# Kernel tuning notes

Measured on AMD Instinct MI355X. Metric: run time of the kernel, lower is better.

Reference implementation:

```python
import jax, jax.numpy as jnp
import numpy as np

N = 2_000_000  # number of Gaussians


def setup_inputs() -> dict:
    key = jax.random.key(0)
    k1, k2, k3 = jax.random.split(key, 3)
    quaternions = jax.random.normal(k1, (N, 4), dtype=jnp.float32)
    scales = jax.random.normal(k2, (N, 3), dtype=jnp.float32) * 0.5
    opacities = jax.random.normal(k3, (N, 1), dtype=jnp.float32)
    return {"quaternions": quaternions, "scales": scales, "opacities": opacities}


def quaternion_to_rotation_matrix(q):
    # q: [N,4] with layout (w, x, y, z) as in the torch source
    w, x, y, z = q[:, 0], q[:, 1], q[:, 2], q[:, 3]
    xx, yy, zz = x * x, y * y, z * z
    xy, xz, yz = x * y, x * z, y * z
    xw, yw, zw = x * w, y * w, z * w
    r0 = jnp.stack([1 - 2 * (yy + zz), 2 * (xy - zw), 2 * (xz + yw)], axis=-1)
    r1 = jnp.stack([2 * (xy + zw), 1 - 2 * (xx + zz), 2 * (yz - xw)], axis=-1)
    r2 = jnp.stack([2 * (xz - yw), 2 * (yz + xw), 1 - 2 * (xx + yy)], axis=-1)
    return jnp.stack([r0, r1, r2], axis=-2)  # [N,3,3]


def reference(quaternions, scales, opacities):
    # sigmoid applied to raw opacities (source: 1/(1+exp(-o)))
    opac = jax.nn.sigmoid(opacities)
    # NOTE: source normalizes by the GLOBAL Frobenius norm of the whole tensor
    # (to.linalg.norm with no dim) -- replicated faithfully.
    qn = quaternions / jnp.linalg.norm(quaternions)
    R = quaternion_to_rotation_matrix(qn)  # [N,3,3]
    # scales_d = (diag(exp(s)))**2 ; scales_i_d = (diag(1/exp(s)))**2
    s2 = jnp.exp(2.0 * scales)      # [N,3] diagonal of S^2
    inv_s2 = jnp.exp(-2.0 * scales)  # [N,3] diagonal of S^-2
    # cov = R @ diag(s2) @ R^T, inv_cov = R @ diag(inv_s2) @ R^T (closed form,
    # no batched 3x3 matmul chain / LAPACK inverse needed)
    cov = jnp.einsum('nij,nj,nkj->nik', R, s2, R)
    inv_cov = jnp.einsum('nij,nj,nkj->nik', R, inv_s2, R)
    return cov, inv_cov, opac
```

## Files before the change

### kernel.cpp

```cpp
#include <hip/hip_runtime.h>
#include <math.h>

#define RBLOCKS 1024
#define RTHREADS 256
#define CHUNK 256

__global__ __launch_bounds__(RTHREADS) void gp_reduce_sq(
    const float4* __restrict__ q4, int n4, double* __restrict__ partials) {
    __shared__ double sdata[RTHREADS];
    double acc = 0.0;
    int stride = gridDim.x * blockDim.x;
    for (int i = blockIdx.x * blockDim.x + threadIdx.x; i < n4; i += stride) {
        float4 v = q4[i];
        acc += (double)v.x * v.x + (double)v.y * v.y +
               (double)v.z * v.z + (double)v.w * v.w;
    }
    sdata[threadIdx.x] = acc;
    __syncthreads();
    for (int s = RTHREADS / 2; s > 0; s >>= 1) {
        if (threadIdx.x < s) sdata[threadIdx.x] += sdata[threadIdx.x + s];
        __syncthreads();
    }
    if (threadIdx.x == 0) partials[blockIdx.x] = sdata[0];
}

__global__ __launch_bounds__(256) void gp_main(
    const float4* __restrict__ q,
    const float* __restrict__ scales,
    const float* __restrict__ opac_in,
    const double* __restrict__ partials,
    float* __restrict__ cov,
    float* __restrict__ inv_cov,
    float* __restrict__ opac_out,
    int n) {
    __shared__ union SU {
        double red[4];
        float mat[2 * CHUNK * 9];
    } u;
    __shared__ float s_sc[CHUNK * 3];

    const int tid = threadIdx.x;
    const int c0 = blockIdx.x * CHUNK;
    const int count = min(CHUNK, n - c0);

    float4 qi = make_float4(0.f, 0.f, 0.f, 0.f);
    float op = 0.f;
    if (tid < count) {
        qi = q[c0 + tid];
        op = opac_in[c0 + tid];
    }
    const int nsf = count * 3;
    const int nsf4 = nsf >> 2;
    const float4* sc4 = (const float4*)(scales + (size_t)c0 * 3);
    float4 sv = make_float4(0.f, 0.f, 0.f, 0.f);
    if (tid < nsf4) sv = sc4[tid];

    double acc = 0.0;
#pragma unroll
    for (int k = 0; k < RBLOCKS / 256; ++k) acc += partials[tid + 256 * k];
#pragma unroll
    for (int off = 32; off > 0; off >>= 1) acc += __shfl_down(acc, off);
    if ((tid & 63) == 0) u.red[tid >> 6] = acc;

    if (tid < nsf4) {
        s_sc[4 * tid + 0] = sv.x;
        s_sc[4 * tid + 1] = sv.y;
        s_sc[4 * tid + 2] = sv.z;
        s_sc[4 * tid + 3] = sv.w;
    }
    {
        int r = nsf - nsf4 * 4;
        if (tid < r) s_sc[nsf4 * 4 + tid] = scales[(size_t)c0 * 3 + nsf4 * 4 + tid];
    }
    __syncthreads();

    double tot = u.red[0] + u.red[1] + u.red[2] + u.red[3];
    const float inv_norm = (float)(1.0 / sqrt(tot));
    __syncthreads();

    if (tid < count) {
        float w = qi.x * inv_norm;
        float x = qi.y * inv_norm;
        float y = qi.z * inv_norm;
        float z = qi.w * inv_norm;

        float xx = x * x, yy = y * y, zz = z * z;
        float xy = x * y, xz = x * z, yz = y * z;
        float xw = x * w, yw = y * w, zw = z * w;

        float r00 = 1.f - 2.f * (yy + zz);
        float r01 = 2.f * (xy - zw);
        float r02 = 2.f * (xz + yw);
        float r10 = 2.f * (xy + zw);
        float r11 = 1.f - 2.f * (xx + zz);
        float r12 = 2.f * (yz - xw);
        float r20 = 2.f * (xz - yw);
        float r21 = 2.f * (yz + xw);
        float r22 = 1.f - 2.f * (xx + yy);

        float s0 = s_sc[3 * tid + 0];
        float s1 = s_sc[3 * tid + 1];
        float s2 = s_sc[3 * tid + 2];

        float e0 = expf(2.f * s0), e1 = expf(2.f * s1), e2 = expf(2.f * s2);
        float f0 = 1.f / e0, f1 = 1.f / e1, f2 = 1.f / e2;

        float* mc = &u.mat[tid * 9];
        float* mi = &u.mat[CHUNK * 9 + tid * 9];
        {
            float a0 = r00 * e0, a1 = r01 * e1, a2 = r02 * e2;
            float b0 = r10 * e0, b1 = r11 * e1, b2 = r12 * e2;
            float c0_ = r20 * e0, c1 = r21 * e1, c2 = r22 * e2;
            float m00 = a0 * r00 + a1 * r01 + a2 * r02;
            float m01 = a0 * r10 + a1 * r11 + a2 * r12;
            float m02 = a0 * r20 + a1 * r21 + a2 * r22;
            float m11 = b0 * r10 + b1 * r11 + b2 * r12;
            float m12 = b0 * r20 + b1 * r21 + b2 * r22;
            float m22 = c0_ * r20 + c1 * r21 + c2 * r22;
            mc[0] = m00; mc[1] = m01; mc[2] = m02;
            mc[3] = m01; mc[4] = m11; mc[5] = m12;
            mc[6] = m02; mc[7] = m12; mc[8] = m22;
        }
        {
            float a0 = r00 * f0, a1 = r01 * f1, a2 = r02 * f2;
            float b0 = r10 * f0, b1 = r11 * f1, b2 = r12 * f2;
            float c0_ = r20 * f0, c1 = r21 * f1, c2 = r22 * f2;
            float m00 = a0 * r00 + a1 * r01 + a2 * r02;
            float m01 = a0 * r10 + a1 * r11 + a2 * r12;
            float m02 = a0 * r20 + a1 * r21 + a2 * r22;
            float m11 = b0 * r10 + b1 * r11 + b2 * r12;
            float m12 = b0 * r20 + b1 * r21 + b2 * r22;
            float m22 = c0_ * r20 + c1 * r21 + c2 * r22;
            mi[0] = m00; mi[1] = m01; mi[2] = m02;
            mi[3] = m01; mi[4] = m11; mi[5] = m12;
            mi[6] = m02; mi[7] = m12; mi[8] = m22;
        }
        opac_out[c0 + tid] = 1.f / (1.f + expf(-op));
    }
    __syncthreads();

    const int nf = count * 9;
    const int nfv = nf >> 2;
    float4* covo = (float4*)(cov + (size_t)c0 * 9);
    float4* invo = (float4*)(inv_cov + (size_t)c0 * 9);
    const float4* mc4 = (const float4*)u.mat;
    const float4* mi4 = (const float4*)(u.mat + CHUNK * 9);
    for (int j = tid; j < nfv; j += 256) covo[j] = mc4[j];
    for (int j = tid; j < nfv; j += 256) invo[j] = mi4[j];
    for (int j = nfv * 4 + tid; j < nf; j += 256) {
        cov[(size_t)c0 * 9 + j] = u.mat[j];
        inv_cov[(size_t)c0 * 9 + j] = u.mat[CHUNK * 9 + j];
    }
}

extern "C" void kernel_launch(void* const* d_in, const int* in_sizes, int n_in,
                              void* d_out, int out_size, void* d_ws, size_t ws_size,
                              hipStream_t stream) {
    const float* q = (const float*)d_in[0];
    const float* scales = (const float*)d_in[1];
    const float* opac = (const float*)d_in[2];
    int n = in_sizes[0] / 4;

    float* out = (float*)d_out;
    float* cov = out;
    float* inv_cov = out + (size_t)n * 9;
    float* opac_out = out + (size_t)n * 18;

    double* partials = (double*)d_ws;

    gp_reduce_sq<<<RBLOCKS, RTHREADS, 0, stream>>>((const float4*)q, n, partials);

    int nblocks = (n + CHUNK - 1) / CHUNK;
    gp_main<<<nblocks, 256, 0, stream>>>(
        (const float4*)q, scales, opac, partials,
        cov, inv_cov, opac_out, n);
}
```

Baseline: 44.72 us.

## Fuse norm reduction and main compute into one cooperative kernel with grid sync

Replaces the two-kernel sequence (global sum-of-squares reduction, then per-chunk covariance compute) with a single persistent cooperative kernel. Each block reduces its share, writes a partial, then a grid-wide sync precedes every block re-reducing the partials and looping over chunks. This removes one kernel launch and its gap, at the cost of grid-sync overhead, a persistent grid bounded by occupancy, and host-side occupancy queries on every call. It falls back to the old two-kernel path if the cooperative launch fails.

```diff
diff --git a/kernel.cpp b/kernel.cpp
--- a/kernel.cpp
+++ b/kernel.cpp
@@ -1,13 +1,167 @@
 #include <hip/hip_runtime.h>
+#include <hip/hip_cooperative_groups.h>
 #include <math.h>
 
+namespace cg = cooperative_groups;
+
+#define BLOCK 256
+#define CHUNK 256
+#define MAXGRID 1024
 #define RBLOCKS 1024
-#define RTHREADS 256
-#define CHUNK 256
-
-__global__ __launch_bounds__(RTHREADS) void gp_reduce_sq(
+
+__global__ __launch_bounds__(BLOCK, 4) void gp_fused(
+    const float4* __restrict__ q,
+    const float* __restrict__ scales,
+    const float* __restrict__ opac_in,
+    double* __restrict__ partials,
+    float* __restrict__ cov,
+    float* __restrict__ inv_cov,
+    float* __restrict__ opac_out,
+    int n) {
+    __shared__ float s_mat[2 * CHUNK * 9];
+    __shared__ float s_sc[CHUNK * 3];
+    __shared__ double s_red[BLOCK / 64];
+
+    const int tid = threadIdx.x;
+    const int nblk = gridDim.x;
+
+    double acc = 0.0;
+    for (int i = blockIdx.x * BLOCK + tid; i < n; i += nblk * BLOCK) {
+        float4 v = q[i];
+        acc += (double)v.x * v.x + (double)v.y * v.y +
+               (double)v.z * v.z + (double)v.w * v.w;
+    }
+#pragma unroll
+    for (int off = 32; off > 0; off >>= 1) acc += __shfl_down(acc, off);
+    if ((tid & 63) == 0) s_red[tid >> 6] = acc;
+    __syncthreads();
+    if (tid == 0)
+        partials[blockIdx.x] = s_red[0] + s_red[1] + s_red[2] + s_red[3];
+
+    cg::this_grid().sync();
+
+    double a2 = 0.0;
+    for (int i = tid; i < nblk; i += BLOCK) a2 += partials[i];
+#pragma unroll
+    for (int off = 32; off > 0; off >>= 1) a2 += __shfl_down(a2, off);
+    __syncthreads();
+    if ((tid & 63) == 0) s_red[tid >> 6] = a2;
+    __syncthreads();
+    const float inv_norm =
+        (float)(1.0 / sqrt(s_red[0] + s_red[1] + s_red[2] + s_red[3]));
+
+    const int nchunks = (n + CHUNK - 1) / CHUNK;
+    for (int c = blockIdx.x; c < nchunks; c += nblk) {
+        const int c0 = c * CHUNK;
+        const int count = min(CHUNK, n - c0);
+
+        __syncthreads();
+
+        const int nsf = count * 3;
+        const int nsf4 = nsf >> 2;
+        const float4* sc4 = (const float4*)(scales + (size_t)c0 * 3);
+        if (tid < nsf4) {
+            float4 sv = sc4[tid];
+            s_sc[4 * tid + 0] = sv.x;
+            s_sc[4 * tid + 1] = sv.y;
+            s_sc[4 * tid + 2] = sv.z;
+            s_sc[4 * tid + 3] = sv.w;
+        }
+        {
+            int r = nsf - (nsf4 << 2);
+            if (tid < r) s_sc[(nsf4 << 2) + tid] =
+                scales[(size_t)c0 * 3 + (nsf4 << 2) + tid];
+        }
+
+        float4 qi = make_float4(0.f, 0.f, 0.f, 0.f);
+        float op = 0.f;
+        if (tid < count) {
+            qi = q[c0 + tid];
+            op = opac_in[c0 + tid];
+        }
+        __syncthreads();
+
+        if (tid < count) {
+            float w = qi.x * inv_norm;
+            float x = qi.y * inv_norm;
+            float y = qi.z * inv_norm;
+            float z = qi.w * inv_norm;
+
+            float xx = x * x, yy = y * y, zz = z * z;
+            float xy = x * y, xz = x * z, yz = y * z;
+            float xw = x * w, yw = y * w, zw = z * w;
+
+            float r00 = 1.f - 2.f * (yy + zz);
+            float r01 = 2.f * (xy - zw);
+            float r02 = 2.f * (xz + yw);
+            float r10 = 2.f * (xy + zw);
+            float r11 = 1.f - 2.f * (xx + zz);
+            float r12 = 2.f * (yz - xw);
+            float r20 = 2.f * (xz - yw);
+            float r21 = 2.f * (yz + xw);
+            float r22 = 1.f - 2.f * (xx + yy);
+
+            float s0 = s_sc[3 * tid + 0];
+            float s1 = s_sc[3 * tid + 1];
+            float s2 = s_sc[3 * tid + 2];
+
+            float e0 = expf(2.f * s0), e1 = expf(2.f * s1), e2 = expf(2.f * s2);
+            float f0 = 1.f / e0, f1 = 1.f / e1, f2 = 1.f / e2;
+
+            float* mc = &s_mat[tid * 9];
+            float* mi = &s_mat[CHUNK * 9 + tid * 9];
+            {
+                float a0 = r00 * e0, a1 = r01 * e1, a2 = r02 * e2;
+                float b0 = r10 * e0, b1 = r11 * e1, b2 = r12 * e2;
+                float g0 = r20 * e0, g1 = r21 * e1, g2 = r22 * e2;
+                float m00 = a0 * r00 + a1 * r01 + a2 * r02;
+                float m01 = a0 * r10 + a1 * r11 + a2 * r12;
+                float m02 = a0 * r20 + a1 * r21 + a2 * r22;
+                float m11 = b0 * r10 + b1 * r11 + b2 * r12;
+                float m12 = b0 * r20 + b1 * r21 + b2 * r22;
+                float m22 = g0 * r20 + g1 * r21 + g2 * r22;
+                mc[0] = m00; mc[1] = m01; mc[2] = m02;
+                mc[3] = m01; mc[4] = m11; mc[5] = m12;
+                mc[6] = m02; mc[7] = m12; mc[8] = m22;
+            }
+            {
+                float a0 = r00 * f0, a1 = r01 * f1, a2 = r02 * f2;
+                float b0 = r10 * f0, b1 = r11 * f1, b2 = r12 * f2;
+                float g0 = r20 * f0, g1 = r21 * f1, g2 = r22 * f2;
+                float m00 = a0 * r00 + a1 * r01 + a2 * r02;
+                float m01 = a0 * r10 + a1 * r11 + a2 * r12;
+                float m02 = a0 * r20 + a1 * r21 + a2 * r22;
+                float m11 = b0 * r10 + b1 * r11 + b2 * r12;
+                float m12 = b0 * r20 + b1 * r21 + b2 * r22;
+                float m22 = g0 * r20 + g1 * r21 + g2 * r22;
+                mi[0] = m00; mi[1] = m01; mi[2] = m02;
+                mi[3] = m01; mi[4] = m11; mi[5] = m12;
+                mi[6] = m02; mi[7] = m12; mi[8] = m22;
+            }
+            opac_out[c0 + tid] = 1.f / (1.f + expf(-op));
+        }
+        __syncthreads();
+
+        const int nf = count * 9;
+        const int nfv = nf >> 2;
+        float4* covo = (float4*)(cov + (size_t)c0 * 9);
+        float4* invo = (float4*)(inv_cov + (size_t)c0 * 9);
+        const float4* mc4 = (const float4*)s_mat;
+        const float4* mi4 = (const float4*)(s_mat + CHUNK * 9);
+        for (int j = tid; j < nfv; j += BLOCK) {
+            covo[j] = mc4[j];
+            invo[j] = mi4[j];
+        }
+        for (int j = (nfv << 2) + tid; j < nf; j += BLOCK) {
+            cov[(size_t)c0 * 9 + j] = s_mat[j];
+            inv_cov[(size_t)c0 * 9 + j] = s_mat[CHUNK * 9 + j];
+        }
+    }
+}
+
+__global__ __launch_bounds__(BLOCK) void gp_reduce_sq(
     const float4* __restrict__ q4, int n4, double* __restrict__ partials) {
-    __shared__ double sdata[RTHREADS];
+    __shared__ double sdata[BLOCK];
     double acc = 0.0;
     int stride = gridDim.x * blockDim.x;
     for (int i = blockIdx.x * blockDim.x + threadIdx.x; i < n4; i += stride) {
@@ -17,14 +171,14 @@
     }
     sdata[threadIdx.x] = acc;
     __syncthreads();
-    for (int s = RTHREADS / 2; s > 0; s >>= 1) {
+    for (int s = BLOCK / 2; s > 0; s >>= 1) {
         if (threadIdx.x < s) sdata[threadIdx.x] += sdata[threadIdx.x + s];
         __syncthreads();
     }
     if (threadIdx.x == 0) partials[blockIdx.x] = sdata[0];
 }
 
-__global__ __launch_bounds__(256) void gp_main(
+__global__ __launch_bounds__(BLOCK) void gp_main(
     const float4* __restrict__ q,
     const float* __restrict__ scales,
     const float* __restrict__ opac_in,
@@ -69,11 +223,11 @@
         s_sc[4 * tid + 3] = sv.w;
     }
     {
-        int r = nsf - nsf4 * 4;
-        if (tid < r) s_sc[nsf4 * 4 + tid] = scales[(size_t)c0 * 3 + nsf4 * 4 + tid];
-    }
-    __syncthreads();
-
+        int r = nsf - (nsf4 << 2);
+        if (tid < r) s_sc[(nsf4 << 2) + tid] =
+            scales[(size_t)c0 * 3 + (nsf4 << 2) + tid];
+    }
+    __syncthreads();
     double tot = u.red[0] + u.red[1] + u.red[2] + u.red[3];
     const float inv_norm = (float)(1.0 / sqrt(tot));
     __syncthreads();
@@ -83,11 +237,9 @@
         float x = qi.y * inv_norm;
         float y = qi.z * inv_norm;
         float z = qi.w * inv_norm;
-
         float xx = x * x, yy = y * y, zz = z * z;
         float xy = x * y, xz = x * z, yz = y * z;
         float xw = x * w, yw = y * w, zw = z * w;
-
         float r00 = 1.f - 2.f * (yy + zz);
         float r01 = 2.f * (xy - zw);
         float r02 = 2.f * (xz + yw);
@@ -97,26 +249,23 @@
         float r20 = 2.f * (xz - yw);
         float r21 = 2.f * (yz + xw);
         float r22 = 1.f - 2.f * (xx + yy);
-
         float s0 = s_sc[3 * tid + 0];
         float s1 = s_sc[3 * tid + 1];
         float s2 = s_sc[3 * tid + 2];
-
         float e0 = expf(2.f * s0), e1 = expf(2.f * s1), e2 = expf(2.f * s2);
         float f0 = 1.f / e0, f1 = 1.f / e1, f2 = 1.f / e2;
-
         float* mc = &u.mat[tid * 9];
         float* mi = &u.mat[CHUNK * 9 + tid * 9];
         {
             float a0 = r00 * e0, a1 = r01 * e1, a2 = r02 * e2;
             float b0 = r10 * e0, b1 = r11 * e1, b2 = r12 * e2;
-            float c0_ = r20 * e0, c1 = r21 * e1, c2 = r22 * e2;
+            float g0 = r20 * e0, g1 = r21 * e1, g2 = r22 * e2;
             float m00 = a0 * r00 + a1 * r01 + a2 * r02;
             float m01 = a0 * r10 + a1 * r11 + a2 * r12;
             float m02 = a0 * r20 + a1 * r21 + a2 * r22;
             float m11 = b0 * r10 + b1 * r11 + b2 * r12;
             float m12 = b0 * r20 + b1 * r21 + b2 * r22;
-            float m22 = c0_ * r20 + c1 * r21 + c2 * r22;
+            float m22 = g0 * r20 + g1 * r21 + g2 * r22;
             mc[0] = m00; mc[1] = m01; mc[2] = m02;
             mc[3] = m01; mc[4] = m11; mc[5] = m12;
             mc[6] = m02; mc[7] = m12; mc[8] = m22;
@@ -124,13 +273,13 @@
         {
             float a0 = r00 * f0, a1 = r01 * f1, a2 = r02 * f2;
             float b0 = r10 * f0, b1 = r11 * f1, b2 = r12 * f2;
-            float c0_ = r20 * f0, c1 = r21 * f1, c2 = r22 * f2;
+            float g0 = r20 * f0, g1 = r21 * f1, g2 = r22 * f2;
             float m00 = a0 * r00 + a1 * r01 + a2 * r02;
             float m01 = a0 * r10 + a1 * r11 + a2 * r12;
             float m02 = a0 * r20 + a1 * r21 + a2 * r22;
             float m11 = b0 * r10 + b1 * r11 + b2 * r12;
             float m12 = b0 * r20 + b1 * r21 + b2 * r22;
-            float m22 = c0_ * r20 + c1 * r21 + c2 * r22;
+            float m22 = g0 * r20 + g1 * r21 + g2 * r22;
             mi[0] = m00; mi[1] = m01; mi[2] = m02;
             mi[3] = m01; mi[4] = m11; mi[5] = m12;
             mi[6] = m02; mi[7] = m12; mi[8] = m22;
@@ -145,9 +294,11 @@
     float4* invo = (float4*)(inv_cov + (size_t)c0 * 9);
     const float4* mc4 = (const float4*)u.mat;
     const float4* mi4 = (const float4*)(u.mat + CHUNK * 9);
-    for (int j = tid; j < nfv; j += 256) covo[j] = mc4[j];
-    for (int j = tid; j < nfv; j += 256) invo[j] = mi4[j];
-    for (int j = nfv * 4 + tid; j < nf; j += 256) {
+    for (int j = tid; j < nfv; j += BLOCK) {
+        covo[j] = mc4[j];
+        invo[j] = mi4[j];
+    }
+    for (int j = (nfv << 2) + tid; j < nf; j += BLOCK) {
         cov[(size_t)c0 * 9 + j] = u.mat[j];
         inv_cov[(size_t)c0 * 9 + j] = u.mat[CHUNK * 9 + j];
     }
@@ -156,7 +307,7 @@
 extern "C" void kernel_launch(void* const* d_in, const int* in_sizes, int n_in,
                               void* d_out, int out_size, void* d_ws, size_t ws_size,
                               hipStream_t stream) {
-    const float* q = (const float*)d_in[0];
+    const float4* q = (const float4*)d_in[0];
     const float* scales = (const float*)d_in[1];
     const float* opac = (const float*)d_in[2];
     int n = in_sizes[0] / 4;
@@ -168,10 +319,31 @@
 
     double* partials = (double*)d_ws;
 
-    gp_reduce_sq<<<RBLOCKS, RTHREADS, 0, stream>>>((const float4*)q, n, partials);
-
-    int nblocks = (n + CHUNK - 1) / CHUNK;
-    gp_main<<<nblocks, 256, 0, stream>>>(
-        (const float4*)q, scales, opac, partials,
-        cov, inv_cov, opac_out, n);
+    int occ = 0;
+    hipError_t qe = hipOccupancyMaxActiveBlocksPerMultiprocessor(
+        &occ, gp_fused, BLOCK, 0);
+    int num_cu = 0;
+    hipError_t ae = hipDeviceGetAttribute(
+        &num_cu, hipDeviceAttributeMultiprocessorCount, 0);
+
+    bool coop_ok = false;
+    if (qe == hipSuccess && ae == hipSuccess && occ > 0 && num_cu > 0) {
+        int grid = occ * num_cu;
+        if (grid > MAXGRID) grid = MAXGRID;
+        if (grid >= 64) {
+            void* args[] = {(void*)&q, (void*)&scales, (void*)&opac,
+                            (void*)&partials, (void*)&cov, (void*)&inv_cov,
+                            (void*)&opac_out, (void*)&n};
+            hipError_t le = hipLaunchCooperativeKernel(
+                (void*)gp_fused, dim3(grid), dim3(BLOCK), args, 0, stream);
+            coop_ok = (le == hipSuccess);
+        }
+    }
+
+    if (!coop_ok) {
+        gp_reduce_sq<<<RBLOCKS, BLOCK, 0, stream>>>(q, n, partials);
+        int nblocks = (n + CHUNK - 1) / CHUNK;
+        gp_main<<<nblocks, BLOCK, 0, stream>>>(
+            q, scales, opac, partials, cov, inv_cov, opac_out, n);
+    }
 }
```

Result: slower. 101.0 us (+125.8%).

## Move sigmoid into reduction pass, use nontemporal stores and fast exp

Applied to the files above, without the earlier changes.

The opacity sigmoid moves out of the main kernel into the first (norm-reduction) pass, which now reads opacities and writes sigmoid outputs alongside its sum of squares. The reduction switches from an LDS tree to wave shuffles. The main kernel loads scales directly per thread instead of staging them in shared memory, uses __expf, and writes cov/inv_cov with nontemporal vector stores. Launch bounds now request higher occupancy. The strided 12-byte per-thread scale loads may coalesce worse than the old float4 staging, and __expf lowers accuracy slightly.

```diff
diff --git a/kernel.cpp b/kernel.cpp
--- a/kernel.cpp
+++ b/kernel.cpp
@@ -1,81 +1,77 @@
 #include <hip/hip_runtime.h>
 #include <math.h>
 
+#define BLOCK 256
+#define CHUNK 256
 #define RBLOCKS 1024
-#define RTHREADS 256
-#define CHUNK 256
 
-__global__ __launch_bounds__(RTHREADS) void gp_reduce_sq(
-    const float4* __restrict__ q4, int n4, double* __restrict__ partials) {
-    __shared__ double sdata[RTHREADS];
+typedef float f32x4 __attribute__((ext_vector_type(4)));
+
+__global__ __launch_bounds__(BLOCK, 4) void gp_pass1(
+    const float4* __restrict__ q4,
+    const float* __restrict__ opac_in,
+    int n,
+    double* __restrict__ partials,
+    float* __restrict__ opac_out) {
+    __shared__ double s_red[BLOCK / 64];
+    const int tid = threadIdx.x;
+    const int stride = gridDim.x * BLOCK;
+
     double acc = 0.0;
-    int stride = gridDim.x * blockDim.x;
-    for (int i = blockIdx.x * blockDim.x + threadIdx.x; i < n4; i += stride) {
+    for (int i = blockIdx.x * BLOCK + tid; i < n; i += stride) {
         float4 v = q4[i];
         acc += (double)v.x * v.x + (double)v.y * v.y +
                (double)v.z * v.z + (double)v.w * v.w;
     }
-    sdata[threadIdx.x] = acc;
+
+    for (int i = blockIdx.x * BLOCK + tid; i < n; i += stride) {
+        float o = __builtin_nontemporal_load(opac_in + i);
+        float r = 1.f / (1.f + __expf(-o));
+        __builtin_nontemporal_store(r, opac_out + i);
+    }
+
+#pragma unroll
+    for (int off = 32; off > 0; off >>= 1) acc += __shfl_down(acc, off);
+    if ((tid & 63) == 0) s_red[tid >> 6] = acc;
     __syncthreads();
-    for (int s = RTHREADS / 2; s > 0; s >>= 1) {
-        if (threadIdx.x < s) sdata[threadIdx.x] += sdata[threadIdx.x + s];
-        __syncthreads();
-    }
-    if (threadIdx.x == 0) partials[blockIdx.x] = sdata[0];
+    if (tid == 0)
+        partials[blockIdx.x] = s_red[0] + s_red[1] + s_red[2] + s_red[3];
 }
 
-__global__ __launch_bounds__(256) void gp_main(
+__global__ __launch_bounds__(BLOCK, 8) void gp_main(
     const float4* __restrict__ q,
     const float* __restrict__ scales,
-    const float* __restrict__ opac_in,
     const double* __restrict__ partials,
     float* __restrict__ cov,
     float* __restrict__ inv_cov,
-    float* __restrict__ opac_out,
     int n) {
     __shared__ union SU {
-        double red[4];
+        double red[BLOCK / 64];
         float mat[2 * CHUNK * 9];
     } u;
-    __shared__ float s_sc[CHUNK * 3];
 
     const int tid = threadIdx.x;
     const int c0 = blockIdx.x * CHUNK;
     const int count = min(CHUNK, n - c0);
 
     float4 qi = make_float4(0.f, 0.f, 0.f, 0.f);
-    float op = 0.f;
+    float s0 = 0.f, s1 = 0.f, s2 = 0.f;
     if (tid < count) {
         qi = q[c0 + tid];
-        op = opac_in[c0 + tid];
+        const float* sc = scales + 3 * (size_t)(c0 + tid);
+        s0 = sc[0];
+        s1 = sc[1];
+        s2 = sc[2];
     }
-    const int nsf = count * 3;
-    const int nsf4 = nsf >> 2;
-    const float4* sc4 = (const float4*)(scales + (size_t)c0 * 3);
-    float4 sv = make_float4(0.f, 0.f, 0.f, 0.f);
-    if (tid < nsf4) sv = sc4[tid];
 
-    double acc = 0.0;
-#pragma unroll
-    for (int k = 0; k < RBLOCKS / 256; ++k) acc += partials[tid + 256 * k];
+    double acc = partials[tid] + partials[tid + 256] +
+                 partials[tid + 512] + partials[tid + 768];
 #pragma unroll
     for (int off = 32; off > 0; off >>= 1) acc += __shfl_down(acc, off);
     if ((tid & 63) == 0) u.red[tid >> 6] = acc;
-
-    if (tid < nsf4) {
-        s_sc[4 * tid + 0] = sv.x;
-        s_sc[4 * tid + 1] = sv.y;
-        s_sc[4 * tid + 2] = sv.z;
-        s_sc[4 * tid + 3] = sv.w;
-    }
-    {
-        int r = nsf - nsf4 * 4;
-        if (tid < r) s_sc[nsf4 * 4 + tid] = scales[(size_t)c0 * 3 + nsf4 * 4 + tid];
-    }
     __syncthreads();
-
-    double tot = u.red[0] + u.red[1] + u.red[2] + u.red[3];
-    const float inv_norm = (float)(1.0 / sqrt(tot));
+    const float inv_norm =
+        (float)(1.0 / sqrt(u.red[0] + u.red[1] + u.red[2] + u.red[3]));
     __syncthreads();
 
     if (tid < count) {
@@ -98,11 +94,7 @@
         float r21 = 2.f * (yz + xw);
         float r22 = 1.f - 2.f * (xx + yy);
 
-        float s0 = s_sc[3 * tid + 0];
-        float s1 = s_sc[3 * tid + 1];
-        float s2 = s_sc[3 * tid + 2];
-
-        float e0 = expf(2.f * s0), e1 = expf(2.f * s1), e2 = expf(2.f * s2);
+        float e0 = __expf(2.f * s0), e1 = __expf(2.f * s1), e2 = __expf(2.f * s2);
         float f0 = 1.f / e0, f1 = 1.f / e1, f2 = 1.f / e2;
 
         float* mc = &u.mat[tid * 9];
@@ -110,13 +102,13 @@
         {
             float a0 = r00 * e0, a1 = r01 * e1, a2 = r02 * e2;
             float b0 = r10 * e0, b1 = r11 * e1, b2 = r12 * e2;
-            float c0_ = r20 * e0, c1 = r21 * e1, c2 = r22 * e2;
+            float g0 = r20 * e0, g1 = r21 * e1, g2 = r22 * e2;
             float m00 = a0 * r00 + a1 * r01 + a2 * r02;
             float m01 = a0 * r10 + a1 * r11 + a2 * r12;
             float m02 = a0 * r20 + a1 * r21 + a2 * r22;
             float m11 = b0 * r10 + b1 * r11 + b2 * r12;
             float m12 = b0 * r20 + b1 * r21 + b2 * r22;
-            float m22 = c0_ * r20 + c1 * r21 + c2 * r22;
+            float m22 = g0 * r20 + g1 * r21 + g2 * r22;
             mc[0] = m00; mc[1] = m01; mc[2] = m02;
             mc[3] = m01; mc[4] = m11; mc[5] = m12;
             mc[6] = m02; mc[7] = m12; mc[8] = m22;
@@ -124,30 +116,31 @@
         {
             float a0 = r00 * f0, a1 = r01 * f1, a2 = r02 * f2;
             float b0 = r10 * f0, b1 = r11 * f1, b2 = r12 * f2;
-            float c0_ = r20 * f0, c1 = r21 * f1, c2 = r22 * f2;
+            float g0 = r20 * f0, g1 = r21 * f1, g2 = r22 * f2;
             float m00 = a0 * r00 + a1 * r01 + a2 * r02;
             float m01 = a0 * r10 + a1 * r11 + a2 * r12;
             float m02 = a0 * r20 + a1 * r21 + a2 * r22;
             float m11 = b0 * r10 + b1 * r11 + b2 * r12;
             float m12 = b0 * r20 + b1 * r21 + b2 * r22;
-            float m22 = c0_ * r20 + c1 * r21 + c2 * r22;
+            float m22 = g0 * r20 + g1 * r21 + g2 * r22;
             mi[0] = m00; mi[1] = m01; mi[2] = m02;
             mi[3] = m01; mi[4] = m11; mi[5] = m12;
             mi[6] = m02; mi[7] = m12; mi[8] = m22;
         }
-        opac_out[c0 + tid] = 1.f / (1.f + expf(-op));
     }
     __syncthreads();
 
     const int nf = count * 9;
     const int nfv = nf >> 2;
-    float4* covo = (float4*)(cov + (size_t)c0 * 9);
-    float4* invo = (float4*)(inv_cov + (size_t)c0 * 9);
-    const float4* mc4 = (const float4*)u.mat;
-    const float4* mi4 = (const float4*)(u.mat + CHUNK * 9);
-    for (int j = tid; j < nfv; j += 256) covo[j] = mc4[j];
-    for (int j = tid; j < nfv; j += 256) invo[j] = mi4[j];
-    for (int j = nfv * 4 + tid; j < nf; j += 256) {
+    f32x4* covo = (f32x4*)(cov + (size_t)c0 * 9);
+    f32x4* invo = (f32x4*)(inv_cov + (size_t)c0 * 9);
+    const f32x4* mc4 = (const f32x4*)u.mat;
+    const f32x4* mi4 = (const f32x4*)(u.mat + CHUNK * 9);
+    for (int j = tid; j < nfv; j += BLOCK) {
+        __builtin_nontemporal_store(mc4[j], covo + j);
+        __builtin_nontemporal_store(mi4[j], invo + j);
+    }
+    for (int j = (nfv << 2) + tid; j < nf; j += BLOCK) {
         cov[(size_t)c0 * 9 + j] = u.mat[j];
         inv_cov[(size_t)c0 * 9 + j] = u.mat[CHUNK * 9 + j];
     }
@@ -156,7 +149,7 @@
 extern "C" void kernel_launch(void* const* d_in, const int* in_sizes, int n_in,
                               void* d_out, int out_size, void* d_ws, size_t ws_size,
                               hipStream_t stream) {
-    const float* q = (const float*)d_in[0];
+    const float4* q = (const float4*)d_in[0];
     const float* scales = (const float*)d_in[1];
     const float* opac = (const float*)d_in[2];
     int n = in_sizes[0] / 4;
@@ -168,10 +161,9 @@
 
     double* partials = (double*)d_ws;
 
-    gp_reduce_sq<<<RBLOCKS, RTHREADS, 0, stream>>>((const float4*)q, n, partials);
+    gp_pass1<<<RBLOCKS, BLOCK, 0, stream>>>(q, opac, n, partials, opac_out);
 
     int nblocks = (n + CHUNK - 1) / CHUNK;
-    gp_main<<<nblocks, 256, 0, stream>>>(
-        (const float4*)q, scales, opac, partials,
-        cov, inv_cov, opac_out, n);
+    gp_main<<<nblocks, BLOCK, 0, stream>>>(
+        q, scales, partials, cov, inv_cov, n);
 }
```

Result: slower. 46.90 us (+4.9%).
